# Kernel tuning notes

Measured on AMD Instinct MI355X. Metric: run time of the kernel, lower is better.

## Reference

```python
import jax, jax.numpy as jnp
import numpy as np

D_MODEL, D_STATE, D_CONV, EXPAND = 1024, 16, 4, 2
D_INNER = D_MODEL * EXPAND
BATCH, SEQ_LEN = 2, 2048
LN_EPS = 1e-5


def setup_inputs() -> dict:
    key = jax.random.key(0)
    ks = jax.random.split(key, 10)
    s = lambda fan_in: 1.0 / np.sqrt(fan_in)
    x = jax.random.normal(ks[0], (BATCH, D_MODEL, SEQ_LEN), jnp.float32)
    ln_w = jnp.ones((D_MODEL,), jnp.float32)
    ln_b = jnp.zeros((D_MODEL,), jnp.float32)
    # Linear weights stored as [in, out]
    W_in = jax.random.normal(ks[1], (D_MODEL, 2 * D_INNER), jnp.float32) * s(D_MODEL)
    conv_w = jax.random.normal(ks[2], (D_INNER, 1, D_CONV), jnp.float32) * s(D_CONV)
    conv_b = jax.random.normal(ks[3], (D_INNER,), jnp.float32) * s(D_CONV)
    W_x = jax.random.normal(ks[4], (D_INNER, 2 * D_STATE + D_INNER), jnp.float32) * s(D_INNER)
    W_dt = jax.random.normal(ks[5], (D_INNER, D_INNER), jnp.float32) * s(D_INNER)
    b_dt = jax.random.normal(ks[6], (D_INNER,), jnp.float32) * s(D_INNER)
    A_log = jnp.broadcast_to(jnp.log(jnp.arange(1, D_STATE + 1, dtype=jnp.float32))[None, :], (D_INNER, D_STATE))
    Dskip = jnp.ones((D_INNER,), jnp.float32)
    W_out = jax.random.normal(ks[7], (D_INNER, D_MODEL), jnp.float32) * s(D_INNER)
    return {"x": x, "ln_w": ln_w, "ln_b": ln_b, "W_in": W_in, "conv_w": conv_w,
            "conv_b": conv_b, "W_x": W_x, "W_dt": W_dt, "b_dt": b_dt,
            "A_log": A_log, "Dskip": Dskip, "W_out": W_out}


def _selective_scan(u, delta, A, Bp, Cp, Dskip):
    # u, delta: [B, d_inner, L]; A: [d_inner, d_state]; Bp, Cp: [B, d_state, L]
    u_T = jnp.transpose(u, (2, 0, 1))        # [L, B, d_inner]
    d_T = jnp.transpose(delta, (2, 0, 1))    # [L, B, d_inner]
    B_T = jnp.transpose(Bp, (2, 0, 1))       # [L, B, d_state]
    C_T = jnp.transpose(Cp, (2, 0, 1))       # [L, B, d_state]
    h0 = jnp.zeros((u.shape[0], u.shape[1], A.shape[1]), u.dtype)

    def step(h, inp):
        dlt_t, B_t, C_t, u_t = inp
        dA = jnp.exp(dlt_t[..., None] * A)                       # [B, d_inner, d_state]
        h = dA * h + dlt_t[..., None] * B_t[:, None, :] * u_t[..., None]
        y_t = jnp.einsum('bds,bs->bd', h, C_t)
        return h, y_t

    _, ys = jax.lax.scan(step, h0, (d_T, B_T, C_T, u_T))
    y = jnp.transpose(ys, (1, 2, 0))  # [B, d_inner, L]
    return y + Dskip[None, :, None] * u


def reference(x, ln_w, ln_b, W_in, conv_w, conv_b, W_x, W_dt, b_dt, A_log, Dskip, W_out):
    residual = x
    xt = jnp.swapaxes(x, 1, 2)  # [B, L, d_model]
    mu = xt.mean(-1, keepdims=True)
    var = ((xt - mu) ** 2).mean(-1, keepdims=True)
    xn = (xt - mu) * jax.lax.rsqrt(var + LN_EPS) * ln_w + ln_b
    xz = xn @ W_in                                   # [B, L, 2*d_inner]
    xb, z = jnp.split(xz, 2, axis=-1)
    xb = jnp.swapaxes(xb, 1, 2)                      # [B, d_inner, L]
    # causal depthwise conv (torch pads d_conv-1 both sides then slices [:L])
    xb = jax.lax.conv_general_dilated(
        xb, conv_w, window_strides=(1,), padding=[(D_CONV - 1, 0)],
        dimension_numbers=('NCH', 'OIH', 'NCH'), feature_group_count=D_INNER)
    xb = xb + conv_b[None, :, None]
    xb = jax.nn.silu(xb)
    xbt = jnp.swapaxes(xb, 1, 2)                     # [B, L, d_inner]
    bcd = xbt @ W_x                                  # [B, L, 2*d_state + d_inner]
    Bp = bcd[..., :D_STATE]
    Cp = bcd[..., D_STATE:2 * D_STATE]
    dlt = jax.nn.softplus(bcd[..., 2 * D_STATE:] @ W_dt + b_dt)
    Bp = jnp.swapaxes(Bp, 1, 2)                      # [B, d_state, L]
    Cp = jnp.swapaxes(Cp, 1, 2)
    dlt = jnp.swapaxes(dlt, 1, 2)                    # [B, d_inner, L]
    A = -jnp.exp(A_log)
    y = _selective_scan(xb, dlt, A, Bp, Cp, Dskip)   # [B, d_inner, L]
    y = jnp.swapaxes(y, 1, 2) * jax.nn.silu(z)       # [B, L, d_inner]
    out = y @ W_out                                  # [B, L, d_model]
    return jnp.swapaxes(out, 1, 2) + residual
```

## Files before the change

kernel.cpp:

```cpp
#include <hip/hip_runtime.h>
#include <cstdint>
#include <cstddef>

#define SEQL 2048
#define DMODEL 1024
#define DINNER 2048
#define NSTATE 16
#define NC 32
#define TC 64
#define KS 16
#define KCH 128

typedef __attribute__((ext_vector_type(4))) float f32x4;
typedef __attribute__((ext_vector_type(8))) short short8;
typedef __attribute__((ext_vector_type(4))) short short4v;
typedef unsigned short u16;

__device__ __forceinline__ float b2f(u16 u) {
  union { unsigned int i; float f; } v; v.i = ((unsigned int)u) << 16; return v.f;
}
__device__ __forceinline__ u16 f2b(float f) {
  union { float f; unsigned int i; } v; v.f = f;
  unsigned int r = v.i + 0x7FFFu + ((v.i >> 16) & 1u);
  return (u16)(r >> 16);
}

__global__ __launch_bounds__(256) void k_transpose_cvt(
    const float* __restrict__ in, u16* __restrict__ out, int R, int C, int c0) {
  __shared__ float t[32][33];
  int cb = blockIdx.x * 32, rb = blockIdx.y * 32;
  int tx = threadIdx.x, ty = threadIdx.y;
#pragma unroll
  for (int i = 0; i < 32; i += 8)
    t[ty + i][tx] = in[(size_t)(rb + ty + i) * C + c0 + cb + tx];
  __syncthreads();
#pragma unroll
  for (int i = 0; i < 32; i += 8)
    out[(size_t)(cb + ty + i) * R + rb + tx] = f2b(t[tx][ty + i]);
}

__global__ __launch_bounds__(256) void k_cvt_rows(
    const float* __restrict__ in, u16* __restrict__ out) {
  size_t idx = (size_t)blockIdx.x * 256 + threadIdx.x;
  size_t i4 = idx * 4;
  int r = (int)(i4 >> 11), c = (int)(i4 & 2047);
  f32x4 v = *(const f32x4*)&in[(size_t)r * 2080 + 32 + c];
  short4v o;
#pragma unroll
  for (int j = 0; j < 4; ++j) o[j] = (short)f2b(v[j]);
  *(short4v*)&out[i4] = o;
}

__global__ __launch_bounds__(256) void k_layernorm(
    const u16* __restrict__ xt, const float* __restrict__ w,
    const float* __restrict__ b, u16* __restrict__ xn) {
  int row = blockIdx.x;
  const u16* px = xt + (size_t)row * DMODEL;
  int i4 = threadIdx.x * 4;
  short4v sv = *(const short4v*)&px[i4];
  float v[4];
#pragma unroll
  for (int j = 0; j < 4; ++j) v[j] = b2f((u16)sv[j]);
  float s1 = v[0] + v[1] + v[2] + v[3];
  float s2 = v[0]*v[0] + v[1]*v[1] + v[2]*v[2] + v[3]*v[3];
#pragma unroll
  for (int off = 32; off > 0; off >>= 1) {
    s1 += __shfl_xor(s1, off);
    s2 += __shfl_xor(s2, off);
  }
  __shared__ float a1[4], a2[4];
  int lane = threadIdx.x & 63, wid = threadIdx.x >> 6;
  if (lane == 0) { a1[wid] = s1; a2[wid] = s2; }
  __syncthreads();
  float t1 = a1[0] + a1[1] + a1[2] + a1[3];
  float t2 = a2[0] + a2[1] + a2[2] + a2[3];
  float mu = t1 * (1.f / DMODEL);
  float rs = rsqrtf(t2 * (1.f / DMODEL) - mu * mu + 1e-5f);
  short4v ov;
#pragma unroll
  for (int j = 0; j < 4; ++j) ov[j] = (short)f2b((v[j] - mu) * rs * w[i4 + j] + b[i4 + j]);
  *(short4v*)&xn[(size_t)row * DMODEL + i4] = ov;
}

__global__ __launch_bounds__(512) void gemm8x(
    const u16* __restrict__ A, const u16* __restrict__ BT,
    u16* __restrict__ outp, int M, int N, int K) {
  constexpr int LDSTILE = 64 * 512;
  __shared__ u16 lds[2 * LDSTILE];

  const int tid = threadIdx.x;
  const int w = tid >> 6, lane = tid & 63;
  const int wm = w >> 2, wn = w & 3;
  const int lg = lane >> 4, lr = lane & 15;
  const int wbase = tid & ~63;

  const int gx = N / 256;
  const int cpx = gridDim.x >> 3;
  const int wg = ((int)blockIdx.x & 7) * cpx + ((int)blockIdx.x >> 3);
  const int tm = (wg / gx) * 256;
  const int tn = (wg % gx) * 256;
  const int NT = K >> 6;

  const u16* Ab = A + (size_t)tm * K;
  const u16* Bb = BT + (size_t)tn * K;

  auto stageA = [&](int tc, int h) {
    int tcl = tc < NT ? tc : NT - 1;
    const u16* g0 = Ab + (size_t)tcl * 64;
    u16* l0 = lds + (tc & 1) * LDSTILE;
#pragma unroll
    for (int j = 0; j < 2; ++j) {
      int t8 = j * 512 + tid;
      int r8 = t8 >> 3;
      int pr = (r8 & 63) + ((r8 >> 6) << 7) + h * 64;
      int sk = ((((t8 & 7) << 4) ^ ((pr & 7) << 4)) >> 1);
      int r8b = (j * 512 + wbase) >> 3;
      int prb = (r8b & 63) + ((r8b >> 6) << 7) + h * 64;
      __builtin_amdgcn_global_load_lds(
          (const __attribute__((address_space(1))) void*)(g0 + (size_t)pr * K + sk),
          (__attribute__((address_space(3))) void*)(l0 + prb * 64), 16, 0, 0);
    }
  };
  auto stageB = [&](int tc, int h) {
    int tcl = tc < NT ? tc : NT - 1;
    const u16* g0 = Bb + (size_t)tcl * 64;
    u16* l0 = lds + (tc & 1) * LDSTILE + 256 * 64;
#pragma unroll
    for (int j = 0; j < 2; ++j) {
      int t8 = j * 512 + tid;
      int r8 = t8 >> 3;
      int pr = (r8 % 32) + (r8 / 32) * 64 + h * 32;
      int sk = ((((t8 & 7) << 4) ^ ((pr & 7) << 4)) >> 1);
      int r8b = (j * 512 + wbase) >> 3;
      int prb = (r8b % 32) + (r8b / 32) * 64 + h * 32;
      __builtin_amdgcn_global_load_lds(
          (const __attribute__((address_space(1))) void*)(g0 + (size_t)pr * K + sk),
          (__attribute__((address_space(3))) void*)(l0 + prb * 64), 16, 0, 0);
    }
  };
  auto fragA = [&](const u16* base, int mf, int kk) -> short8 {
    int r = wm * 128 + mf * 16 + lr;
    int cb = (kk * 64 + lg * 16) ^ ((r & 7) << 4);
    return *(const short8*)((const char*)base + r * 128 + cb);
  };
  auto fragB = [&](const u16* base, int nf, int kk) -> short8 {
    int r = wn * 64 + nf * 16 + lr;
    int cb = (kk * 64 + lg * 16) ^ ((r & 7) << 4);
    return *(const short8*)((const char*)base + 256 * 128 + r * 128 + cb);
  };

  f32x4 acc[8][4] = {};
  short8 aF[4][2], bF0[2][2], bF1[2][2];

  stageA(0, 0); stageB(0, 0); stageB(0, 1); stageA(0, 1);
  stageA(1, 0); stageB(1, 0);
  asm volatile("s_waitcnt vmcnt(4)" ::: "memory");
  __builtin_amdgcn_s_barrier();

  for (int t = 0; t < NT; ++t) {
    const u16* Ac = lds + (t & 1) * LDSTILE;
#pragma unroll
    for (int mf = 0; mf < 4; ++mf) { aF[mf][0] = fragA(Ac, mf, 0); aF[mf][1] = fragA(Ac, mf, 1); }
#pragma unroll
    for (int nf = 0; nf < 2; ++nf) { bF0[nf][0] = fragB(Ac, nf, 0); bF0[nf][1] = fragB(Ac, nf, 1); }
    stageB(t + 1, 1);
    __builtin_amdgcn_s_barrier();
    asm volatile("s_waitcnt lgkmcnt(0)" ::: "memory");
    __builtin_amdgcn_s_setprio(1);
#pragma unroll
    for (int mf = 0; mf < 4; ++mf)
#pragma unroll
      for (int nf = 0; nf < 2; ++nf) {
        acc[mf][nf] = __builtin_amdgcn_mfma_f32_16x16x32_bf16(aF[mf][0], bF0[nf][0], acc[mf][nf], 0, 0, 0);
        acc[mf][nf] = __builtin_amdgcn_mfma_f32_16x16x32_bf16(aF[mf][1], bF0[nf][1], acc[mf][nf], 0, 0, 0);
      }
    __builtin_amdgcn_s_setprio(0);
    __builtin_amdgcn_s_barrier();
#pragma unroll
    for (int nf = 0; nf < 2; ++nf) { bF1[nf][0] = fragB(Ac, 2 + nf, 0); bF1[nf][1] = fragB(Ac, 2 + nf, 1); }
    stageA(t + 1, 1);
    __builtin_amdgcn_s_barrier();
    asm volatile("s_waitcnt lgkmcnt(0)" ::: "memory");
    __builtin_amdgcn_s_setprio(1);
#pragma unroll
    for (int mf = 0; mf < 4; ++mf)
#pragma unroll
      for (int nf = 0; nf < 2; ++nf) {
        acc[mf][2 + nf] = __builtin_amdgcn_mfma_f32_16x16x32_bf16(aF[mf][0], bF1[nf][0], acc[mf][2 + nf], 0, 0, 0);
        acc[mf][2 + nf] = __builtin_amdgcn_mfma_f32_16x16x32_bf16(aF[mf][1], bF1[nf][1], acc[mf][2 + nf], 0, 0, 0);
      }
    __builtin_amdgcn_s_setprio(0);
    __builtin_amdgcn_s_barrier();
#pragma unroll
    for (int mf = 0; mf < 4; ++mf) { aF[mf][0] = fragA(Ac, 4 + mf, 0); aF[mf][1] = fragA(Ac, 4 + mf, 1); }
    stageA(t + 2, 0);
    __builtin_amdgcn_s_barrier();
    asm volatile("s_waitcnt lgkmcnt(0)" ::: "memory");
    __builtin_amdgcn_s_setprio(1);
#pragma unroll
    for (int mf = 0; mf < 4; ++mf)
#pragma unroll
      for (int nf = 0; nf < 2; ++nf) {
        acc[4 + mf][nf] = __builtin_amdgcn_mfma_f32_16x16x32_bf16(aF[mf][0], bF0[nf][0], acc[4 + mf][nf], 0, 0, 0);
        acc[4 + mf][nf] = __builtin_amdgcn_mfma_f32_16x16x32_bf16(aF[mf][1], bF0[nf][1], acc[4 + mf][nf], 0, 0, 0);
      }
    __builtin_amdgcn_s_setprio(0);
    __builtin_amdgcn_s_barrier();
    stageB(t + 2, 0);
    __builtin_amdgcn_s_barrier();
    asm volatile("s_waitcnt lgkmcnt(0)" ::: "memory");
    __builtin_amdgcn_s_setprio(1);
#pragma unroll
    for (int mf = 0; mf < 4; ++mf)
#pragma unroll
      for (int nf = 0; nf < 2; ++nf) {
        acc[4 + mf][2 + nf] = __builtin_amdgcn_mfma_f32_16x16x32_bf16(aF[mf][0], bF1[nf][0], acc[4 + mf][2 + nf], 0, 0, 0);
        acc[4 + mf][2 + nf] = __builtin_amdgcn_mfma_f32_16x16x32_bf16(aF[mf][1], bF1[nf][1], acc[4 + mf][2 + nf], 0, 0, 0);
      }
    __builtin_amdgcn_s_setprio(0);
    asm volatile("s_waitcnt vmcnt(4)" ::: "memory");
    __builtin_amdgcn_s_barrier();
  }

#pragma unroll
  for (int mf = 0; mf < 8; ++mf) {
    int r0 = tm + wm * 128 + mf * 16 + lg * 4;
#pragma unroll
    for (int nf = 0; nf < 4; ++nf) {
      int c = tn + wn * 64 + nf * 16 + lr;
      f32x4 v = acc[mf][nf];
#pragma unroll
      for (int j = 0; j < 4; ++j)
        outp[(size_t)(r0 + j) * N + c] = f2b(v[j]);
    }
  }
}

template<int EPI>
__global__ __launch_bounds__(256) void gemm8p(
    const u16* __restrict__ A, const u16* __restrict__ BT,
    void* __restrict__ outp, const float* __restrict__ bias,
    const float* __restrict__ resid, int M, int N, int K) {
  constexpr int LDSTILE = 2 * 128 * 64;
  __shared__ u16 lds[2 * LDSTILE];

  const int tid = threadIdx.x;
  const int w = tid >> 6, lane = tid & 63;
  const int wm = w >> 1, wn = w & 1;
  const int lg = lane >> 4, lr = lane & 15;
  const int wbase = tid & ~63;

  const int gx = N / 128;
  const int cpx = gridDim.x >> 3;
  const int wg = ((int)blockIdx.x & 7) * cpx + ((int)blockIdx.x >> 3);
  const int tm = (wg / gx) * 128;
  const int tn = (wg % gx) * 128;
  const int NT = K >> 6;

  const u16* aSp[2];
  const u16* bSp[2];
  int aD[2], bD[2];
#pragma unroll
  for (int j = 0; j < 2; ++j) {
    int t8 = j * 256 + tid;
    int r8 = t8 >> 3;
    int pr = (r8 & 31) + ((r8 >> 5) << 6);
    int sk = ((((t8 & 7) << 4) ^ ((pr & 7) << 4)) >> 1);
    aSp[j] = A + (size_t)(tm + pr) * K + sk;
    bSp[j] = BT + (size_t)(tn + pr) * K + sk;
    int r8b = (j * 256 + wbase) >> 3;
    int prb = (r8b & 31) + ((r8b >> 5) << 6);
    aD[j] = prb * 64;
    bD[j] = 128 * 64 + prb * 64;
  }
  int aFo[4][2], bFo[4][2];
#pragma unroll
  for (int mf = 0; mf < 4; ++mf)
#pragma unroll
    for (int kk = 0; kk < 2; ++kk) {
      int r = wm * 64 + mf * 16 + lr;
      aFo[mf][kk] = r * 128 + ((kk * 64 + lg * 16) ^ ((r & 7) << 4));
      int rb = wn * 64 + mf * 16 + lr;
      bFo[mf][kk] = 128 * 64 * 2 + rb * 128 + ((kk * 64 + lg * 16) ^ ((rb & 7) << 4));
    }

  auto stA = [&](int toff, int h, int buf) {
#pragma unroll
    for (int j = 0; j < 2; ++j)
      __builtin_amdgcn_global_load_lds(
          (const __attribute__((address_space(1))) void*)(aSp[j] + toff * 64 + h * (K << 5)),
          (__attribute__((address_space(3))) void*)(lds + buf * LDSTILE + aD[j] + h * 2048),
          16, 0, 0);
  };
  auto stB = [&](int toff, int h, int buf) {
#pragma unroll
    for (int j = 0; j < 2; ++j)
      __builtin_amdgcn_global_load_lds(
          (const __attribute__((address_space(1))) void*)(bSp[j] + toff * 64 + h * (K << 5)),
          (__attribute__((address_space(3))) void*)(lds + buf * LDSTILE + bD[j] + h * 2048),
          16, 0, 0);
  };

  f32x4 acc[4][4] = {};
  short8 aF[2][2], bF0[2][2], bF1[2][2];

  stA(0, 0, 0); stB(0, 0, 0); stB(0, 1, 0); stA(0, 1, 0);
  stA(1, 0, 1); stB(1, 0, 1);
  asm volatile("s_waitcnt vmcnt(4)" ::: "memory");
  __builtin_amdgcn_s_barrier();

  for (int tt = 0; tt < NT; tt += 2) {
#pragma unroll
    for (int u = 0; u < 2; ++u) {
      const char* Lb = (const char*)lds + u * (LDSTILE * 2);
#pragma unroll
      for (int mf = 0; mf < 2; ++mf)
#pragma unroll
        for (int kk = 0; kk < 2; ++kk) aF[mf][kk] = *(const short8*)(Lb + aFo[mf][kk]);
#pragma unroll
      for (int nf = 0; nf < 2; ++nf)
#pragma unroll
        for (int kk = 0; kk < 2; ++kk) bF0[nf][kk] = *(const short8*)(Lb + bFo[nf][kk]);
      stB(u + 1, 1, (u + 1) & 1);
      __builtin_amdgcn_s_barrier();
      asm volatile("s_waitcnt lgkmcnt(0)" ::: "memory");
      __builtin_amdgcn_s_setprio(1);
#pragma unroll
      for (int mf = 0; mf < 2; ++mf)
#pragma unroll
        for (int nf = 0; nf < 2; ++nf) {
          acc[mf][nf] = __builtin_amdgcn_mfma_f32_16x16x32_bf16(aF[mf][0], bF0[nf][0], acc[mf][nf], 0, 0, 0);
          acc[mf][nf] = __builtin_amdgcn_mfma_f32_16x16x32_bf16(aF[mf][1], bF0[nf][1], acc[mf][nf], 0, 0, 0);
        }
      __builtin_amdgcn_s_setprio(0);
      __builtin_amdgcn_s_barrier();
#pragma unroll
      for (int nf = 0; nf < 2; ++nf)
#pragma unroll
        for (int kk = 0; kk < 2; ++kk) bF1[nf][kk] = *(const short8*)(Lb + bFo[2 + nf][kk]);
      stA(u + 1, 1, (u + 1) & 1);
      __builtin_amdgcn_s_barrier();
      asm volatile("s_waitcnt lgkmcnt(0)" ::: "memory");
      __builtin_amdgcn_s_setprio(1);
#pragma unroll
      for (int mf = 0; mf < 2; ++mf)
#pragma unroll
        for (int nf = 0; nf < 2; ++nf) {
          acc[mf][2 + nf] = __builtin_amdgcn_mfma_f32_16x16x32_bf16(aF[mf][0], bF1[nf][0], acc[mf][2 + nf], 0, 0, 0);
          acc[mf][2 + nf] = __builtin_amdgcn_mfma_f32_16x16x32_bf16(aF[mf][1], bF1[nf][1], acc[mf][2 + nf], 0, 0, 0);
        }
      __builtin_amdgcn_s_setprio(0);
      __builtin_amdgcn_s_barrier();
#pragma unroll
      for (int mf = 0; mf < 2; ++mf)
#pragma unroll
        for (int kk = 0; kk < 2; ++kk) aF[mf][kk] = *(const short8*)(Lb + aFo[2 + mf][kk]);
      stA(u + 2, 0, u & 1);
      __builtin_amdgcn_s_barrier();
      asm volatile("s_waitcnt lgkmcnt(0)" ::: "memory");
      __builtin_amdgcn_s_setprio(1);
#pragma unroll
      for (int mf = 0; mf < 2; ++mf)
#pragma unroll
        for (int nf = 0; nf < 2; ++nf) {
          acc[2 + mf][nf] = __builtin_amdgcn_mfma_f32_16x16x32_bf16(aF[mf][0], bF0[nf][0], acc[2 + mf][nf], 0, 0, 0);
          acc[2 + mf][nf] = __builtin_amdgcn_mfma_f32_16x16x32_bf16(aF[mf][1], bF0[nf][1], acc[2 + mf][nf], 0, 0, 0);
        }
      __builtin_amdgcn_s_setprio(0);
      __builtin_amdgcn_s_barrier();
      stB(u + 2, 0, u & 1);
      __builtin_amdgcn_s_barrier();
      asm volatile("s_waitcnt lgkmcnt(0)" ::: "memory");
      __builtin_amdgcn_s_setprio(1);
#pragma unroll
      for (int mf = 0; mf < 2; ++mf)
#pragma unroll
        for (int nf = 0; nf < 2; ++nf) {
          acc[2 + mf][2 + nf] = __builtin_amdgcn_mfma_f32_16x16x32_bf16(aF[mf][0], bF1[nf][0], acc[2 + mf][2 + nf], 0, 0, 0);
          acc[2 + mf][2 + nf] = __builtin_amdgcn_mfma_f32_16x16x32_bf16(aF[mf][1], bF1[nf][1], acc[2 + mf][2 + nf], 0, 0, 0);
        }
      __builtin_amdgcn_s_setprio(0);
      asm volatile("s_waitcnt vmcnt(4)" ::: "memory");
      __builtin_amdgcn_s_barrier();
    }
#pragma unroll
    for (int j = 0; j < 2; ++j) { aSp[j] += 128; bSp[j] += 128; }
  }

#pragma unroll
  for (int mf = 0; mf < 4; ++mf) {
    int r0 = tm + wm * 64 + mf * 16 + lg * 4;
#pragma unroll
    for (int nf = 0; nf < 4; ++nf) {
      int c2 = tn + wn * 64 + nf * 16 + lr;
      f32x4 v = acc[mf][nf];
#pragma unroll
      for (int j = 0; j < 4; ++j) {
        int r = r0 + j;
        if constexpr (EPI == 1) {
          ((u16*)outp)[(size_t)r * N + c2] = f2b(v[j]);
        } else if constexpr (EPI == 2) {
          float xv = v[j] + bias[c2];
          float sp = (xv > 20.f) ? xv : log1pf(__expf(xv));
          ((u16*)outp)[(size_t)r * N + c2] = f2b(sp);
        } else if constexpr (EPI == 3) {
          int bb = r >> 11, tt2 = r & (SEQL - 1);
          size_t oi = ((size_t)(bb * N + c2)) * SEQL + tt2;
          ((float*)outp)[oi] = v[j] + resid[oi];
        } else {
          ((float*)outp)[(size_t)r * N + c2] = v[j];
        }
      }
    }
  }
}

__global__ __launch_bounds__(256) void k_conv_silu(
    const u16* __restrict__ xz, const float* __restrict__ cw,
    const float* __restrict__ cb, u16* __restrict__ xbt) {
  size_t idx = (size_t)blockIdx.x * 256 + threadIdx.x;
  int d2 = (int)(idx & (DINNER / 2 - 1));
  int d = d2 * 2;
  int l = (int)((idx >> 10) & (SEQL - 1));
  int b = (int)(idx >> 21);
  f32x4 w0 = *(const f32x4*)&cw[d * 4];
  f32x4 w1 = *(const f32x4*)&cw[d * 4 + 4];
  float a0 = cb[d], a1 = cb[d + 1];
  size_t base = ((size_t)b * SEQL + l) * 4096 + d;
#pragma unroll
  for (int i = 0; i < 4; ++i) {
    int ls = l - 3 + i;
    if (ls >= 0) {
      unsigned int pv = *(const unsigned int*)&xz[base + (size_t)(i - 3) * 4096];
      a0 += w0[i] * b2f((u16)(pv & 0xFFFF));
      a1 += w1[i] * b2f((u16)(pv >> 16));
    }
  }
  float s0 = a0 / (1.f + __expf(-a0));
  float s1 = a1 / (1.f + __expf(-a1));
  unsigned int ov = (unsigned int)f2b(s0) | ((unsigned int)f2b(s1) << 16);
  *(unsigned int*)&xbt[((size_t)b * SEQL + l) * DINNER + d] = ov;
}

__global__ __launch_bounds__(256) void k_bc_mfma(
    const u16* __restrict__ xbt, const u16* __restrict__ WxBCT,
    float* __restrict__ bcp) {
  __shared__ u16 As[128 * 32];
  int tid = threadIdx.x;
  int w = tid >> 6, lane = tid & 63;
  int tm = blockIdx.x * 128;
  int k0 = blockIdx.y * KCH;
  int lg = lane >> 4, lr = lane & 15;
  int srow = lane >> 2, scol = (lane & 3) * 8;

  f32x4 acc[2][2] = {};

  for (int kk = k0; kk < k0 + KCH; kk += 32) {
#pragma unroll
    for (int j = 0; j < 2; ++j) {
      int ch = w * 2 + j;
      const u16* ga = xbt + (size_t)(tm + ch * 16 + srow) * DINNER + kk + scol;
      __builtin_amdgcn_global_load_lds(
          (const __attribute__((address_space(1))) void*)ga,
          (__attribute__((address_space(3))) void*)&As[ch * 512], 16, 0, 0);
    }
    __syncthreads();
    short8 aF[2], bF[2];
#pragma unroll
    for (int m = 0; m < 2; ++m)
      aF[m] = *(const short8*)&As[(w * 32 + m * 16 + lr) * 32 + lg * 8];
#pragma unroll
    for (int n = 0; n < 2; ++n)
      bF[n] = *(const short8*)&WxBCT[(size_t)(n * 16 + lr) * DINNER + kk + lg * 8];
#pragma unroll
    for (int m = 0; m < 2; ++m)
#pragma unroll
      for (int n = 0; n < 2; ++n)
        acc[m][n] = __builtin_amdgcn_mfma_f32_16x16x32_bf16(aF[m], bF[n], acc[m][n], 0, 0, 0);
    __syncthreads();
  }

  float* outp = bcp + (size_t)blockIdx.y * (4096 * 32);
#pragma unroll
  for (int m = 0; m < 2; ++m) {
    int r0 = tm + w * 32 + m * 16 + lg * 4;
#pragma unroll
    for (int n = 0; n < 2; ++n) {
      int c = n * 16 + lr;
      f32x4 v = acc[m][n];
#pragma unroll
      for (int j = 0; j < 4; ++j)
        outp[(size_t)(r0 + j) * 32 + c] = v[j];
    }
  }
}

__global__ __launch_bounds__(256) void k_bc_red(
    const float* __restrict__ bcp, float* __restrict__ bc) {
  size_t i = (size_t)blockIdx.x * 256 + threadIdx.x;
  float s = 0.f;
#pragma unroll
  for (int ks = 0; ks < KS; ++ks)
    s += bcp[(size_t)ks * (4096 * 32) + i];
  bc[i] = s;
}

__global__ __launch_bounds__(256) void k_scan_p1(
    const u16* __restrict__ dlt, const u16* __restrict__ ub,
    const float* __restrict__ bcv, const float* __restrict__ A_log,
    float* __restrict__ Pc, float* __restrict__ Qc) {
  int d = blockIdx.x * 256 + threadIdx.x;
  int c = blockIdx.y;
  int b = blockIdx.z;
  float Av[16];
#pragma unroll
  for (int sv = 0; sv < 4; ++sv) {
    f32x4 al = *(const f32x4*)&A_log[d * 16 + sv * 4];
#pragma unroll
    for (int j = 0; j < 4; ++j) Av[sv * 4 + j] = -__expf(al[j]);
  }
  float P[16], Q[16];
#pragma unroll
  for (int s = 0; s < 16; ++s) { P[s] = 1.f; Q[s] = 0.f; }
  size_t row0 = (size_t)b * SEQL + (size_t)c * TC;
  for (int t = 0; t < TC; ++t) {
    size_t row = row0 + t;
    float dl = b2f(dlt[row * DINNER + d]);
    float uu = b2f(ub[row * DINNER + d]);
    float bco = dl * uu;
    const f32x4* Bp = (const f32x4*)&bcv[row * 32];
#pragma unroll
    for (int sv = 0; sv < 4; ++sv) {
      f32x4 Bv = Bp[sv];
#pragma unroll
      for (int j = 0; j < 4; ++j) {
        int s = sv * 4 + j;
        float dA = __expf(dl * Av[s]);
        P[s] *= dA;
        Q[s] = dA * Q[s] + bco * Bv[j];
      }
    }
  }
  size_t base = (((size_t)b * NC + c) * DINNER + d) * 16;
#pragma unroll
  for (int sv = 0; sv < 4; ++sv) {
    f32x4 pv, qv;
#pragma unroll
    for (int j = 0; j < 4; ++j) { pv[j] = P[sv * 4 + j]; qv[j] = Q[sv * 4 + j]; }
    *(f32x4*)&Pc[base + sv * 4] = pv;
    *(f32x4*)&Qc[base + sv * 4] = qv;
  }
}

__global__ __launch_bounds__(256) void k_scan_p2(
    const float* __restrict__ Pc, const float* __restrict__ Qc,
    float* __restrict__ Hs) {
  size_t gid = (size_t)blockIdx.x * 256 + threadIdx.x;
  size_t bds = gid & ((size_t)DINNER * 16 - 1);
  int b = (int)(gid >> 15);
  float h = 0.f;
  size_t cstride = (size_t)DINNER * 16;
  size_t base = (size_t)b * NC * cstride + bds;
  for (int c = 0; c < NC; ++c) {
    size_t idx = base + (size_t)c * cstride;
    Hs[idx] = h;
    h = Pc[idx] * h + Qc[idx];
  }
}

__global__ __launch_bounds__(256) void k_scan_p3(
    const u16* __restrict__ dlt, const u16* __restrict__ ub,
    const float* __restrict__ bcv, const u16* __restrict__ xz,
    const float* __restrict__ A_log, const float* __restrict__ Dskip,
    const float* __restrict__ Hs, u16* __restrict__ yg) {
  int d = blockIdx.x * 256 + threadIdx.x;
  int c = blockIdx.y;
  int b = blockIdx.z;
  float Av[16];
#pragma unroll
  for (int sv = 0; sv < 4; ++sv) {
    f32x4 al = *(const f32x4*)&A_log[d * 16 + sv * 4];
#pragma unroll
    for (int j = 0; j < 4; ++j) Av[sv * 4 + j] = -__expf(al[j]);
  }
  float h[16];
  size_t hb = (((size_t)b * NC + c) * DINNER + d) * 16;
#pragma unroll
  for (int sv = 0; sv < 4; ++sv) {
    f32x4 hv = *(const f32x4*)&Hs[hb + sv * 4];
#pragma unroll
    for (int j = 0; j < 4; ++j) h[sv * 4 + j] = hv[j];
  }
  float Dsk = Dskip[d];
  size_t row0 = (size_t)b * SEQL + (size_t)c * TC;
  for (int t = 0; t < TC; ++t) {
    size_t row = row0 + t;
    float dl = b2f(dlt[row * DINNER + d]);
    float uu = b2f(ub[row * DINNER + d]);
    float bco = dl * uu;
    const f32x4* BCp = (const f32x4*)&bcv[row * 32];
    float y = 0.f;
#pragma unroll
    for (int sv = 0; sv < 4; ++sv) {
      f32x4 Bv = BCp[sv];
      f32x4 Cv = BCp[4 + sv];
#pragma unroll
      for (int j = 0; j < 4; ++j) {
        int s = sv * 4 + j;
        float dA = __expf(dl * Av[s]);
        h[s] = dA * h[s] + bco * Bv[j];
        y += h[s] * Cv[j];
      }
    }
    float zv = b2f(xz[row * 4096 + DINNER + d]);
    float yv = (y + Dsk * uu) * (zv / (1.f + __expf(-zv)));
    yg[row * DINNER + d] = f2b(yv);
  }
}

extern "C" void kernel_launch(void* const* d_in, const int* in_sizes, int n_in,
                              void* d_out, int out_size, void* d_ws, size_t ws_size,
                              hipStream_t stream) {
  (void)in_sizes; (void)n_in; (void)out_size; (void)ws_size;
  const float* x      = (const float*)d_in[0];
  const float* ln_w   = (const float*)d_in[1];
  const float* ln_b   = (const float*)d_in[2];
  const float* W_in   = (const float*)d_in[3];
  const float* conv_w = (const float*)d_in[4];
  const float* conv_b = (const float*)d_in[5];
  const float* W_x    = (const float*)d_in[6];
  const float* W_dt   = (const float*)d_in[7];
  const float* b_dt   = (const float*)d_in[8];
  const float* A_log  = (const float*)d_in[9];
  const float* Dskip  = (const float*)d_in[10];
  const float* W_out  = (const float*)d_in[11];
  float* out = (float*)d_out;

  char* ws = (char*)d_ws;
  const size_t MB = 1048576;
  u16*  xt    = (u16*)(ws + 0 * MB);
  u16*  xn    = (u16*)(ws + 8 * MB);
  u16*  WinT  = (u16*)(ws + 16 * MB);
  u16*  WdtT  = (u16*)(ws + 32 * MB);
  u16*  WoutT = (u16*)(ws + 40 * MB);
  u16*  xz    = (u16*)(ws + 44 * MB);
  u16*  xbt   = (u16*)(ws + 76 * MB);
  float* bc   = (float*)(ws + 92 * MB);
  u16*  WxRaw = (u16*)(ws + 93 * MB);
  u16*  W_cT  = (u16*)(ws + 101 * MB);
  u16*  dlt   = (u16*)(ws + 109 * MB);
  float* Pc   = (float*)(ws + 141 * MB);
  float* Qc   = (float*)(ws + 149 * MB);
  float* Hs   = (float*)(ws + 157 * MB);
  float* bcp  = (float*)(ws + 165 * MB);
  u16*  WxBCT = (u16*)(ws + 173 * MB);
  u16*  yg    = (u16*)(ws + 0 * MB);

  dim3 tb(32, 8);
  for (int b = 0; b < 2; ++b)
    k_transpose_cvt<<<dim3(SEQL / 32, DMODEL / 32), tb, 0, stream>>>(
        x + (size_t)b * DMODEL * SEQL, xt + (size_t)b * SEQL * DMODEL, DMODEL, SEQL, 0);
  k_transpose_cvt<<<dim3(4096 / 32, 1024 / 32), tb, 0, stream>>>(W_in, WinT, 1024, 4096, 0);
  k_transpose_cvt<<<dim3(1, 2048 / 32), tb, 0, stream>>>(W_x, WxBCT, 2048, 2080, 0);
  k_transpose_cvt<<<dim3(2048 / 32, 2048 / 32), tb, 0, stream>>>(W_dt, WdtT, 2048, 2048, 0);
  k_transpose_cvt<<<dim3(1024 / 32, 2048 / 32), tb, 0, stream>>>(W_out, WoutT, 2048, 1024, 0);
  k_cvt_rows<<<4096, 256, 0, stream>>>(W_x, WxRaw);

  gemm8p<1><<<256, 256, 0, stream>>>(WdtT, WxRaw, W_cT, nullptr, nullptr, 2048, 2048, 2048);

  k_layernorm<<<4096, 256, 0, stream>>>(xt, ln_w, ln_b, xn);

  gemm8x<<<256, 512, 0, stream>>>(xn, WinT, xz, 4096, 4096, 1024);

  k_conv_silu<<<16384, 256, 0, stream>>>(xz, conv_w, conv_b, xbt);

  k_bc_mfma<<<dim3(4096 / 128, KS), 256, 0, stream>>>(xbt, WxBCT, bcp);
  k_bc_red<<<131072 / 256, 256, 0, stream>>>(bcp, bc);

  gemm8p<2><<<512, 256, 0, stream>>>(xbt, W_cT, dlt, b_dt, nullptr, 4096, 2048, 2048);

  k_scan_p1<<<dim3(DINNER / 256, NC, 2), 256, 0, stream>>>(dlt, xbt, bc, A_log, Pc, Qc);
  k_scan_p2<<<256, 256, 0, stream>>>(Pc, Qc, Hs);
  k_scan_p3<<<dim3(DINNER / 256, NC, 2), 256, 0, stream>>>(
      dlt, xbt, bc, xz, A_log, Dskip, Hs, yg);

  gemm8p<3><<<256, 256, 0, stream>>>(yg, WoutT, out, nullptr, x, 4096, 1024, 2048);
}
```

Before: 306.3 us.

## Fuse B/C projection into delta GEMM and swap operands of output GEMM

Appends the 32 B/C projection columns of W_x to the fused dt weight matrix, padded to N=2176. One GEMM now produces both softplus(delta) and the fp32 B/C values, which removes the split-K bc kernel and its reduction pass. The output projection GEMM is also recast as W_out^T x y^T, so its epilogue writes directly into the [B, d_model, L] layout with coalesced stores along L. The cost is some wasted padded columns in the GEMM. The padding rows of W_aug beyond 2080 are never written and may hold stale data, but their results are discarded.

```diff
diff --git a/kernel.cpp b/kernel.cpp
--- a/kernel.cpp
+++ b/kernel.cpp
@@ -8,8 +8,6 @@
 #define NSTATE 16
 #define NC 32
 #define TC 64
-#define KS 16
-#define KCH 128
 
 typedef __attribute__((ext_vector_type(4))) float f32x4;
 typedef __attribute__((ext_vector_type(8))) short short8;
@@ -399,16 +397,18 @@
         int r = r0 + j;
         if constexpr (EPI == 1) {
           ((u16*)outp)[(size_t)r * N + c2] = f2b(v[j]);
-        } else if constexpr (EPI == 2) {
-          float xv = v[j] + bias[c2];
-          float sp = (xv > 20.f) ? xv : log1pf(__expf(xv));
-          ((u16*)outp)[(size_t)r * N + c2] = f2b(sp);
-        } else if constexpr (EPI == 3) {
-          int bb = r >> 11, tt2 = r & (SEQL - 1);
-          size_t oi = ((size_t)(bb * N + c2)) * SEQL + tt2;
+        } else if constexpr (EPI == 4) {
+          int bb = c2 >> 11, t = c2 & (SEQL - 1);
+          size_t oi = ((size_t)(bb * 1024 + r)) * SEQL + t;
           ((float*)outp)[oi] = v[j] + resid[oi];
-        } else {
-          ((float*)outp)[(size_t)r * N + c2] = v[j];
+        } else if constexpr (EPI == 5) {
+          if (c2 < 2048) {
+            float xv = v[j] + bias[c2];
+            float sp = (xv > 20.f) ? xv : log1pf(__expf(xv));
+            ((u16*)outp)[(size_t)r * 2048 + c2] = f2b(sp);
+          } else if (c2 < 2080) {
+            ((float*)const_cast<float*>(resid))[(size_t)r * 32 + (c2 - 2048)] = v[j];
+          }
         }
       }
     }
@@ -440,69 +440,6 @@
   float s1 = a1 / (1.f + __expf(-a1));
   unsigned int ov = (unsigned int)f2b(s0) | ((unsigned int)f2b(s1) << 16);
   *(unsigned int*)&xbt[((size_t)b * SEQL + l) * DINNER + d] = ov;
-}
-
-__global__ __launch_bounds__(256) void k_bc_mfma(
-    const u16* __restrict__ xbt, const u16* __restrict__ WxBCT,
-    float* __restrict__ bcp) {
-  __shared__ u16 As[128 * 32];
-  int tid = threadIdx.x;
-  int w = tid >> 6, lane = tid & 63;
-  int tm = blockIdx.x * 128;
-  int k0 = blockIdx.y * KCH;
-  int lg = lane >> 4, lr = lane & 15;
-  int srow = lane >> 2, scol = (lane & 3) * 8;
-
-  f32x4 acc[2][2] = {};
-
-  for (int kk = k0; kk < k0 + KCH; kk += 32) {
-#pragma unroll
-    for (int j = 0; j < 2; ++j) {
-      int ch = w * 2 + j;
-      const u16* ga = xbt + (size_t)(tm + ch * 16 + srow) * DINNER + kk + scol;
-      __builtin_amdgcn_global_load_lds(
-          (const __attribute__((address_space(1))) void*)ga,
-          (__attribute__((address_space(3))) void*)&As[ch * 512], 16, 0, 0);
-    }
-    __syncthreads();
-    short8 aF[2], bF[2];
-#pragma unroll
-    for (int m = 0; m < 2; ++m)
-      aF[m] = *(const short8*)&As[(w * 32 + m * 16 + lr) * 32 + lg * 8];
-#pragma unroll
-    for (int n = 0; n < 2; ++n)
-      bF[n] = *(const short8*)&WxBCT[(size_t)(n * 16 + lr) * DINNER + kk + lg * 8];
-#pragma unroll
-    for (int m = 0; m < 2; ++m)
-#pragma unroll
-      for (int n = 0; n < 2; ++n)
-        acc[m][n] = __builtin_amdgcn_mfma_f32_16x16x32_bf16(aF[m], bF[n], acc[m][n], 0, 0, 0);
-    __syncthreads();
-  }
-
-  float* outp = bcp + (size_t)blockIdx.y * (4096 * 32);
-#pragma unroll
-  for (int m = 0; m < 2; ++m) {
-    int r0 = tm + w * 32 + m * 16 + lg * 4;
-#pragma unroll
-    for (int n = 0; n < 2; ++n) {
-      int c = n * 16 + lr;
-      f32x4 v = acc[m][n];
-#pragma unroll
-      for (int j = 0; j < 4; ++j)
-        outp[(size_t)(r0 + j) * 32 + c] = v[j];
-    }
-  }
-}
-
-__global__ __launch_bounds__(256) void k_bc_red(
-    const float* __restrict__ bcp, float* __restrict__ bc) {
-  size_t i = (size_t)blockIdx.x * 256 + threadIdx.x;
-  float s = 0.f;
-#pragma unroll
-  for (int ks = 0; ks < KS; ++ks)
-    s += bcp[(size_t)ks * (4096 * 32) + i];
-  bc[i] = s;
 }
 
 __global__ __launch_bounds__(256) void k_scan_p1(
@@ -647,13 +584,11 @@
   u16*  xbt   = (u16*)(ws + 76 * MB);
   float* bc   = (float*)(ws + 92 * MB);
   u16*  WxRaw = (u16*)(ws + 93 * MB);
-  u16*  W_cT  = (u16*)(ws + 101 * MB);
-  u16*  dlt   = (u16*)(ws + 109 * MB);
+  u16*  W_aug = (u16*)(ws + 101 * MB);
+  u16*  dlt   = (u16*)(ws + 110 * MB);
   float* Pc   = (float*)(ws + 141 * MB);
   float* Qc   = (float*)(ws + 149 * MB);
   float* Hs   = (float*)(ws + 157 * MB);
-  float* bcp  = (float*)(ws + 165 * MB);
-  u16*  WxBCT = (u16*)(ws + 173 * MB);
   u16*  yg    = (u16*)(ws + 0 * MB);
 
   dim3 tb(32, 8);
@@ -661,12 +596,12 @@
     k_transpose_cvt<<<dim3(SEQL / 32, DMODEL / 32), tb, 0, stream>>>(
         x + (size_t)b * DMODEL * SEQL, xt + (size_t)b * SEQL * DMODEL, DMODEL, SEQL, 0);
   k_transpose_cvt<<<dim3(4096 / 32, 1024 / 32), tb, 0, stream>>>(W_in, WinT, 1024, 4096, 0);
-  k_transpose_cvt<<<dim3(1, 2048 / 32), tb, 0, stream>>>(W_x, WxBCT, 2048, 2080, 0);
   k_transpose_cvt<<<dim3(2048 / 32, 2048 / 32), tb, 0, stream>>>(W_dt, WdtT, 2048, 2048, 0);
   k_transpose_cvt<<<dim3(1024 / 32, 2048 / 32), tb, 0, stream>>>(W_out, WoutT, 2048, 1024, 0);
   k_cvt_rows<<<4096, 256, 0, stream>>>(W_x, WxRaw);
-
-  gemm8p<1><<<256, 256, 0, stream>>>(WdtT, WxRaw, W_cT, nullptr, nullptr, 2048, 2048, 2048);
+  k_transpose_cvt<<<dim3(1, 2048 / 32), tb, 0, stream>>>(W_x, W_aug + (size_t)2048 * 2048, 2048, 2080, 0);
+
+  gemm8p<1><<<256, 256, 0, stream>>>(WdtT, WxRaw, W_aug, nullptr, nullptr, 2048, 2048, 2048);
 
   k_layernorm<<<4096, 256, 0, stream>>>(xt, ln_w, ln_b, xn);
 
@@ -674,15 +609,12 @@
 
   k_conv_silu<<<16384, 256, 0, stream>>>(xz, conv_w, conv_b, xbt);
 
-  k_bc_mfma<<<dim3(4096 / 128, KS), 256, 0, stream>>>(xbt, WxBCT, bcp);
-  k_bc_red<<<131072 / 256, 256, 0, stream>>>(bcp, bc);
-
-  gemm8p<2><<<512, 256, 0, stream>>>(xbt, W_cT, dlt, b_dt, nullptr, 4096, 2048, 2048);
+  gemm8p<5><<<544, 256, 0, stream>>>(xbt, W_aug, dlt, b_dt, bc, 4096, 2176, 2048);
 
   k_scan_p1<<<dim3(DINNER / 256, NC, 2), 256, 0, stream>>>(dlt, xbt, bc, A_log, Pc, Qc);
   k_scan_p2<<<256, 256, 0, stream>>>(Pc, Qc, Hs);
   k_scan_p3<<<dim3(DINNER / 256, NC, 2), 256, 0, stream>>>(
       dlt, xbt, bc, xz, A_log, Dskip, Hs, yg);
 
-  gemm8p<3><<<256, 256, 0, stream>>>(yg, WoutT, out, nullptr, x, 4096, 1024, 2048);
-}
+  gemm8p<4><<<256, 256, 0, stream>>>(WoutT, yg, out, nullptr, x, 1024, 4096, 2048);
+}
```

New measurement: 327.2 us. 6.8% more time.
